# Kernel tuning notes

Measured on AMD Instinct MI355X. Metric: run time of the kernel, lower is better.

Reference implementation:

```python
import jax, jax.numpy as jnp
import numpy as np

N = 100000      # nodes
E = 1600000     # edges
G = 1024        # graphs in batch
NF = 9          # atom features (OGB AtomEncoder)
V = 128         # vocab per atom feature
H = 128         # hidden_dim
L = 3           # num_graph_layers
OUT = 10        # output_dim
BN_EPS = 1e-5


def setup_inputs() -> dict:
    key = jax.random.key(0)
    ks = jax.random.split(key, 12)
    x = jax.random.randint(ks[0], (N, NF), 0, V, dtype=jnp.int32)
    edge_index = jax.random.randint(ks[1], (2, E), 0, N, dtype=jnp.int32)
    batch = jnp.sort(jax.random.randint(ks[2], (N,), 0, G, dtype=jnp.int32))
    emb = jax.random.normal(ks[3], (NF, V, H), dtype=jnp.float32) * 0.05
    Ws = jax.random.normal(ks[4], (L, H, H), dtype=jnp.float32) * (1.0 / np.sqrt(H))
    bs = jnp.zeros((L, H), dtype=jnp.float32)
    gamma = jnp.ones((L - 1, H), dtype=jnp.float32)
    beta = jnp.zeros((L - 1, H), dtype=jnp.float32)
    run_mean = jax.random.normal(ks[5], (L - 1, H), dtype=jnp.float32) * 0.1
    run_var = jax.random.uniform(ks[6], (L - 1, H), minval=0.5, maxval=1.5, dtype=jnp.float32)
    W_clf = jax.random.normal(ks[7], (H, OUT), dtype=jnp.float32) * (1.0 / np.sqrt(H))
    b_clf = jnp.zeros((OUT,), dtype=jnp.float32)
    return {"x": x, "edge_index": edge_index, "batch": batch, "emb": emb,
            "Ws": Ws, "bs": bs, "gamma": gamma, "beta": beta,
            "run_mean": run_mean, "run_var": run_var,
            "W_clf": W_clf, "b_clf": b_clf}


def reference(x, edge_index, batch, emb, Ws, bs, gamma, beta, run_mean, run_var, W_clf, b_clf):
    # Eval-mode forward: dropout = identity, BatchNorm uses running stats.
    src, dst = edge_index[0], edge_index[1]
    # GCN symmetric normalization with self-loops: deg = 1 + in-degree
    deg = jax.ops.segment_sum(jnp.ones((E,), jnp.float32), dst, num_segments=N) + 1.0
    dinv = jax.lax.rsqrt(deg)                 # [N]
    norm_e = dinv[src] * dinv[dst]            # [E] edge coefficient
    norm_self = dinv * dinv                   # [N] self-loop coefficient

    # AtomEncoder: sum of per-feature embedding lookups -> [N, H]
    h = emb[jnp.arange(NF)[None, :], x].sum(axis=1)

    for i in range(L):
        hw = h @ Ws[i]                                                       # [N, H]
        h = (jax.ops.segment_sum(hw[src] * norm_e[:, None], dst, num_segments=N)
             + hw * norm_self[:, None] + bs[i])                              # GCNConv
        if i < L - 1:
            h = (h - run_mean[i]) * (gamma[i] * jax.lax.rsqrt(run_var[i] + BN_EPS)) + beta[i]
            h = jax.nn.relu(h)

    # global mean pool over graphs
    counts = jax.ops.segment_sum(jnp.ones((N,), jnp.float32), batch, num_segments=G)
    pooled = jax.ops.segment_sum(h, batch, num_segments=G) / jnp.maximum(counts, 1.0)[:, None]
    return pooled @ W_clf + b_clf             # [G, OUT]
```

## Files before the change

### kernel.cpp

```cpp
#include <hip/hip_runtime.h>
#include <hip/hip_bf16.h>
#include <hip/hip_fp16.h>

#define NN 100000
#define EE 1600000
#define GG 1024
#define NF 9
#define VV 128
#define HH 128
#define LL 3
#define OUTD 10
#define BN_EPS 1e-5f
#define NBUCK 196
#define BCAP 12288
#define CHUNK 4096
#define NSPLIT 391
#define NENC 3125
#define NB128 782

typedef __attribute__((ext_vector_type(8))) short short8;
typedef __attribute__((ext_vector_type(4))) float f32x4;

__device__ inline unsigned short f2bf(float x) {
    unsigned u = __float_as_uint(x);
    unsigned r = (u + 0x7fffu + ((u >> 16) & 1u)) >> 16;
    return (unsigned short)r;
}
__device__ inline float bf2f(unsigned short b) { return __uint_as_float(((unsigned)b) << 16); }

__device__ inline void mix8(float a[8], const uint4& r, float nm) {
    asm("v_fma_mix_f32 %0, %8, %12, %0 op_sel:[0,0,0] op_sel_hi:[1,0,0]\n\t"
        "v_fma_mix_f32 %1, %8, %12, %1 op_sel:[1,0,0] op_sel_hi:[1,0,0]\n\t"
        "v_fma_mix_f32 %2, %9, %12, %2 op_sel:[0,0,0] op_sel_hi:[1,0,0]\n\t"
        "v_fma_mix_f32 %3, %9, %12, %3 op_sel:[1,0,0] op_sel_hi:[1,0,0]\n\t"
        "v_fma_mix_f32 %4, %10, %12, %4 op_sel:[0,0,0] op_sel_hi:[1,0,0]\n\t"
        "v_fma_mix_f32 %5, %10, %12, %5 op_sel:[1,0,0] op_sel_hi:[1,0,0]\n\t"
        "v_fma_mix_f32 %6, %11, %12, %6 op_sel:[0,0,0] op_sel_hi:[1,0,0]\n\t"
        "v_fma_mix_f32 %7, %11, %12, %7 op_sel:[1,0,0] op_sel_hi:[1,0,0]"
        : "+v"(a[0]), "+v"(a[1]), "+v"(a[2]), "+v"(a[3]),
          "+v"(a[4]), "+v"(a[5]), "+v"(a[6]), "+v"(a[7])
        : "v"(r.x), "v"(r.y), "v"(r.z), "v"(r.w), "v"(nm));
}

__global__ __launch_bounds__(256) void wprep_kernel(const float* __restrict__ Ws,
        const float* __restrict__ Wc, const float* __restrict__ b2,
        unsigned short* __restrict__ WThi, unsigned short* __restrict__ WTlo,
        unsigned short* __restrict__ WcThi, unsigned short* __restrict__ WcTlo,
        float* __restrict__ bb2, int* __restrict__ bcur, float* __restrict__ pooled) {
    int id = blockIdx.x * 256 + threadIdx.x;
    if (id < LL * HH * HH) {
        int layer = id >> 14;
        int rem = id & (HH * HH - 1);
        int k = rem >> 7, n = rem & 127;
        float w = Ws[id];
        unsigned short hi = f2bf(w);
        float lo = w - bf2f(hi);
        WThi[(size_t)layer * HH * HH + n * HH + k] = hi;
        WTlo[(size_t)layer * HH * HH + n * HH + k] = f2bf(lo);
    }
    int tid = threadIdx.x;
    if (blockIdx.x == 0) {
        const float* W2 = Ws + (size_t)2 * HH * HH;
        for (int i = tid; i < 16 * HH; i += 256) {
            int n = i >> 7, k = i & 127;
            float s = 0.f;
            if (n < OUTD) {
                for (int j = 0; j < HH; ++j)
                    s += W2[k * HH + j] * Wc[j * OUTD + n];
            }
            unsigned short hi = f2bf(s);
            WcThi[i] = hi;
            WcTlo[i] = f2bf(s - bf2f(hi));
        }
        if (tid < OUTD) {
            float s = 0.f;
            for (int c = 0; c < HH; ++c) s += b2[c] * Wc[c * OUTD + tid];
            bb2[tid] = s;
        }
    } else if (blockIdx.x == 1) {
        bcur[tid] = 0;
    } else if (blockIdx.x >= 2 && blockIdx.x < 66) {
        pooled[(blockIdx.x - 2) * 256 + tid] = 0.f;
    }
}

__global__ __launch_bounds__(256) void split_enc_kernel(
        const int* __restrict__ src, const int* __restrict__ dst,
        int* __restrict__ bcur, int* __restrict__ bucket_edges,
        const int* __restrict__ x, const float* __restrict__ emb,
        const unsigned short* __restrict__ WThi, const unsigned short* __restrict__ WTlo,
        __half* __restrict__ hw_out) {
    __shared__ __align__(16) char smem_raw[25600];
    int tid = threadIdx.x;
    if (blockIdx.x < NSPLIT) {
        int* lcnt  = (int*)smem_raw;
        int* loff  = lcnt + 256;
        int* lcur  = loff + 256;
        int* gbase = lcur + 256;
        int* sh    = gbase + 256;
        int* stage = sh + 256;
        unsigned char* stageb = (unsigned char*)(stage + CHUNK);
        int cs = blockIdx.x * CHUNK;
        int n = min(CHUNK, EE - cs);
        lcnt[tid] = 0;
        __syncthreads();
        for (int i = tid; i < n; i += 256)
            atomicAdd(&lcnt[dst[cs + i] >> 9], 1);
        __syncthreads();
        int val = lcnt[tid];
        sh[tid] = val; __syncthreads();
        for (int d = 1; d < 256; d <<= 1) {
            int t = (tid >= d) ? sh[tid - d] : 0;
            __syncthreads();
            sh[tid] += t;
            __syncthreads();
        }
        loff[tid] = sh[tid] - val;
        lcur[tid] = sh[tid] - val;
        __syncthreads();
        for (int i = tid; i < n; i += 256) {
            int d = dst[cs + i], s = src[cs + i];
            int b = d >> 9;
            int p = atomicAdd(&lcur[b], 1);
            stage[p] = (s << 9) | (d & 511);
            stageb[p] = (unsigned char)b;
        }
        if (val > 0) gbase[tid] = atomicAdd(&bcur[tid], val);
        __syncthreads();
        for (int i = tid; i < n; i += 256) {
            int b = stageb[i];
            bucket_edges[(size_t)b * BCAP + gbase[b] + (i - loff[b])] = stage[i];
        }
    } else {
        unsigned short (*lh)[136] = (unsigned short(*)[136])smem_raw;
        unsigned short (*ll)[136] = (unsigned short(*)[136])(smem_raw + 32 * 136 * 2);
        int nloc = tid >> 3;
        int seg = tid & 7;
        int nodebase = (blockIdx.x - NSPLIT) * 32;
        int n = nodebase + nloc;
        float s[16];
#pragma unroll
        for (int i = 0; i < 16; ++i) s[i] = 0.f;
#pragma unroll
        for (int f = 0; f < NF; ++f) {
            int idx = x[n * NF + f];
            const float4* ep = (const float4*)(emb + ((size_t)(f * VV + idx)) * HH + seg * 16);
#pragma unroll
            for (int q = 0; q < 4; ++q) {
                float4 e = ep[q];
                s[q * 4 + 0] += e.x; s[q * 4 + 1] += e.y;
                s[q * 4 + 2] += e.z; s[q * 4 + 3] += e.w;
            }
        }
#pragma unroll
        for (int q = 0; q < 4; ++q) {
            ushort4 oh, ol;
            oh.x = f2bf(s[q * 4 + 0]); ol.x = f2bf(s[q * 4 + 0] - bf2f(oh.x));
            oh.y = f2bf(s[q * 4 + 1]); ol.y = f2bf(s[q * 4 + 1] - bf2f(oh.y));
            oh.z = f2bf(s[q * 4 + 2]); ol.z = f2bf(s[q * 4 + 2] - bf2f(oh.z));
            oh.w = f2bf(s[q * 4 + 3]); ol.w = f2bf(s[q * 4 + 3] - bf2f(oh.w));
            *(ushort4*)&lh[nloc][seg * 16 + q * 4] = oh;
            *(ushort4*)&ll[nloc][seg * 16 + q * 4] = ol;
        }
        __syncthreads();
        int wave = tid >> 6, lane = tid & 63;
        int quad = lane >> 4, m = lane & 15;
        f32x4 acc[2][2] = {};
        int kq = quad * 8;
#pragma unroll
        for (int t = 0; t < 4; ++t) {
            int k0 = t * 32 + kq;
            short8 a0h = *(const short8*)&lh[m][k0];
            short8 a0l = *(const short8*)&ll[m][k0];
            short8 a1h = *(const short8*)&lh[16 + m][k0];
            short8 a1l = *(const short8*)&ll[16 + m][k0];
#pragma unroll
            for (int c = 0; c < 2; ++c) {
                int ct = wave * 2 + c;
                short8 bh = *(const short8*)(WThi + (size_t)(ct * 16 + m) * HH + k0);
                short8 bl = *(const short8*)(WTlo + (size_t)(ct * 16 + m) * HH + k0);
                acc[0][c] = __builtin_amdgcn_mfma_f32_16x16x32_bf16(a0h, bh, acc[0][c], 0, 0, 0);
                acc[0][c] = __builtin_amdgcn_mfma_f32_16x16x32_bf16(a0l, bh, acc[0][c], 0, 0, 0);
                acc[0][c] = __builtin_amdgcn_mfma_f32_16x16x32_bf16(a0h, bl, acc[0][c], 0, 0, 0);
                acc[1][c] = __builtin_amdgcn_mfma_f32_16x16x32_bf16(a1h, bh, acc[1][c], 0, 0, 0);
                acc[1][c] = __builtin_amdgcn_mfma_f32_16x16x32_bf16(a1l, bh, acc[1][c], 0, 0, 0);
                acc[1][c] = __builtin_amdgcn_mfma_f32_16x16x32_bf16(a1h, bl, acc[1][c], 0, 0, 0);
            }
        }
#pragma unroll
        for (int c = 0; c < 2; ++c) {
            int colx = (wave * 2 + c) * 16 + m;
#pragma unroll
            for (int rt = 0; rt < 2; ++rt) {
                int r0 = nodebase + rt * 16 + quad * 4;
#pragma unroll
                for (int reg = 0; reg < 4; ++reg)
                    hw_out[(size_t)(r0 + reg) * HH + colx] = __float2half(acc[rt][c][reg]);
            }
        }
    }
}

__global__ __launch_bounds__(256) void bhist_kernel(const int* __restrict__ bcur,
                                                    const int* __restrict__ bucket_edges,
                                                    int* __restrict__ cnt,
                                                    float* __restrict__ dinv,
                                                    int* __restrict__ bsum) {
    __shared__ int lc[512];
    __shared__ int sh[256];
    int b = blockIdx.x, tid = threadIdx.x;
    lc[tid] = 0; lc[tid + 256] = 0;
    __syncthreads();
    int n = bcur[b];
    const int* be = bucket_edges + (size_t)b * BCAP;
    for (int i = tid; i < n; i += 256) atomicAdd(&lc[be[i] & 511], 1);
    __syncthreads();
    int node = b * 512 + tid;
    int c0 = lc[tid], c1 = lc[tid + 256];
    int s = 0;
    if (node < NN) { cnt[node] = c0; dinv[node] = rsqrtf(1.0f + (float)c0); s += c0; }
    if (node + 256 < NN) { cnt[node + 256] = c1; dinv[node + 256] = rsqrtf(1.0f + (float)c1); s += c1; }
    sh[tid] = s; __syncthreads();
    for (int d = 128; d > 0; d >>= 1) { if (tid < d) sh[tid] += sh[tid + d]; __syncthreads(); }
    if (tid == 0) bsum[b] = sh[0];
}

__global__ void scanC_kernel(const int* __restrict__ cnt, const int* __restrict__ bsum,
                             int* __restrict__ row_ptr) {
    __shared__ int sh[256];
    __shared__ int pre[256];
    int tid = threadIdx.x;
    pre[tid] = (tid < blockIdx.x && tid < NBUCK) ? bsum[tid] : 0;
    __syncthreads();
    for (int d = 128; d > 0; d >>= 1) { if (tid < d) pre[tid] += pre[tid + d]; __syncthreads(); }
    int bbase = pre[0];
    int base = blockIdx.x * 512 + tid * 2;
    int v0 = (base < NN) ? cnt[base] : 0;
    int v1 = (base + 1 < NN) ? cnt[base + 1] : 0;
    int ts = v0 + v1;
    sh[tid] = ts; __syncthreads();
    for (int d = 1; d < 256; d <<= 1) {
        int t = (tid >= d) ? sh[tid - d] : 0;
        __syncthreads();
        sh[tid] += t;
        __syncthreads();
    }
    int excl = sh[tid] - ts + bbase;
    if (base < NN) row_ptr[base] = excl;
    if (base + 1 < NN) row_ptr[base + 1] = excl + v0;
    if (blockIdx.x == 0 && tid == 0) row_ptr[NN] = EE;
}

__global__ __launch_bounds__(256) void cscatter_kernel(const int* __restrict__ bcur,
                                                       const int* __restrict__ bucket_edges,
                                                       const int* __restrict__ row_ptr,
                                                       const float* __restrict__ dinv,
                                                       int2* __restrict__ col) {
    __shared__ int lcur[512];
    int b = blockIdx.x, tid = threadIdx.x;
    int node0 = b * 512;
#pragma unroll
    for (int k = 0; k < 2; ++k) {
        int j = tid + k * 256;
        int node = node0 + j;
        if (node < NN) lcur[j] = row_ptr[node];
    }
    __syncthreads();
    int n = bcur[b];
    const int* be = bucket_edges + (size_t)b * BCAP;
    for (int i = tid; i < n; i += 256) {
        int w = be[i];
        int j = w & 511;
        int s = (int)((unsigned)w >> 9);
        int p = atomicAdd(&lcur[j], 1);
        float nm = dinv[s] * dinv[node0 + j];
        col[p] = make_int2(s, __float_as_int(nm));
    }
}

__device__ inline void gather_node(const uint4* __restrict__ hw4,
                                   const int2* __restrict__ col,
                                   int start, int end, int c4,
                                   float a[8], float b[8]) {
    int e = start;
    for (; e + 4 <= end; e += 4) {
        unsigned long long w0 = *(const unsigned long long*)&col[e];
        unsigned long long w1 = *(const unsigned long long*)&col[e + 1];
        unsigned long long w2 = *(const unsigned long long*)&col[e + 2];
        unsigned long long w3 = *(const unsigned long long*)&col[e + 3];
        uint4 r0 = hw4[(size_t)(unsigned)(w0 & 0xffffffffu) * 16 + c4];
        uint4 r1 = hw4[(size_t)(unsigned)(w1 & 0xffffffffu) * 16 + c4];
        uint4 r2 = hw4[(size_t)(unsigned)(w2 & 0xffffffffu) * 16 + c4];
        uint4 r3 = hw4[(size_t)(unsigned)(w3 & 0xffffffffu) * 16 + c4];
        mix8(a, r0, __int_as_float((int)(unsigned)(w0 >> 32)));
        mix8(b, r1, __int_as_float((int)(unsigned)(w1 >> 32)));
        mix8(a, r2, __int_as_float((int)(unsigned)(w2 >> 32)));
        mix8(b, r3, __int_as_float((int)(unsigned)(w3 >> 32)));
    }
    if (e < end) {
        int last = end - 1;
        int e1 = min(e + 1, last), e2 = min(e + 2, last), e3 = min(e + 3, last);
        unsigned long long w0 = *(const unsigned long long*)&col[e];
        unsigned long long w1 = *(const unsigned long long*)&col[e1];
        unsigned long long w2 = *(const unsigned long long*)&col[e2];
        unsigned long long w3 = *(const unsigned long long*)&col[e3];
        float n0 = __int_as_float((int)(unsigned)(w0 >> 32));
        float n1 = (e + 1 < end) ? __int_as_float((int)(unsigned)(w1 >> 32)) : 0.f;
        float n2 = (e + 2 < end) ? __int_as_float((int)(unsigned)(w2 >> 32)) : 0.f;
        float n3 = (e + 3 < end) ? __int_as_float((int)(unsigned)(w3 >> 32)) : 0.f;
        uint4 r0 = hw4[(size_t)(unsigned)(w0 & 0xffffffffu) * 16 + c4];
        uint4 r1 = hw4[(size_t)(unsigned)(w1 & 0xffffffffu) * 16 + c4];
        uint4 r2 = hw4[(size_t)(unsigned)(w2 & 0xffffffffu) * 16 + c4];
        uint4 r3 = hw4[(size_t)(unsigned)(w3 & 0xffffffffu) * 16 + c4];
        mix8(a, r0, n0);
        mix8(b, r1, n1);
        mix8(a, r2, n2);
        mix8(b, r3, n3);
    }
}

template<bool DO_PROJ>
__global__ __launch_bounds__(512) void agg_mm_kernel(const __half* __restrict__ hw_in,
    const int* __restrict__ row_ptr, const int2* __restrict__ col,
    const float* __restrict__ dinv,
    const float* __restrict__ bias, const float* __restrict__ gamma,
    const float* __restrict__ beta, const float* __restrict__ rmean,
    const float* __restrict__ rvar,
    const unsigned short* __restrict__ WThi, const unsigned short* __restrict__ WTlo,
    __half* __restrict__ hw_out,
    const unsigned short* __restrict__ WcThi, const unsigned short* __restrict__ WcTlo,
    __half* __restrict__ y_out) {
    __shared__ __align__(16) unsigned short lh[32][136];
    __shared__ __align__(16) unsigned short ll[32][136];
    int wave = threadIdx.x >> 6;
    int lane = threadIdx.x & 63;
    int grp = lane >> 4;
    int c4 = lane & 15;
    int nodebase = blockIdx.x * 32;
    const uint4* hw4 = (const uint4*)hw_in;

    int v = nodebase + wave * 4 + grp;
    int start = row_ptr[v], end = row_ptr[v + 1];
    float a[8] = {}, b[8] = {};
    gather_node(hw4, col, start, end, c4, a, b);

    {
        float dv = dinv[v];
        uint4 r = hw4[(size_t)v * 16 + c4];
        mix8(a, r, dv * dv);
    }
#pragma unroll
    for (int i = 0; i < 8; ++i) a[i] += b[i];

    int ch = c4 * 8;
#pragma unroll
    for (int i = 0; i < 8; ++i) a[i] += bias[ch + i];
#pragma unroll
    for (int i = 0; i < 8; ++i) {
        int c = ch + i;
        float sc = gamma[c] * rsqrtf(rvar[c] + BN_EPS);
        a[i] = fmaxf((a[i] - rmean[c]) * sc + beta[c], 0.f);
    }
    int rloc = wave * 4 + grp;
    ushort4 oh0, oh1, ol0, ol1;
    oh0.x = f2bf(a[0]); ol0.x = f2bf(a[0] - bf2f(oh0.x));
    oh0.y = f2bf(a[1]); ol0.y = f2bf(a[1] - bf2f(oh0.y));
    oh0.z = f2bf(a[2]); ol0.z = f2bf(a[2] - bf2f(oh0.z));
    oh0.w = f2bf(a[3]); ol0.w = f2bf(a[3] - bf2f(oh0.w));
    oh1.x = f2bf(a[4]); ol1.x = f2bf(a[4] - bf2f(oh1.x));
    oh1.y = f2bf(a[5]); ol1.y = f2bf(a[5] - bf2f(oh1.y));
    oh1.z = f2bf(a[6]); ol1.z = f2bf(a[6] - bf2f(oh1.z));
    oh1.w = f2bf(a[7]); ol1.w = f2bf(a[7] - bf2f(oh1.w));
    *(ushort4*)&lh[rloc][ch]     = oh0;
    *(ushort4*)&lh[rloc][ch + 4] = oh1;
    *(ushort4*)&ll[rloc][ch]     = ol0;
    *(ushort4*)&ll[rloc][ch + 4] = ol1;

    __syncthreads();
    int quad = lane >> 4, m = lane & 15;
    f32x4 acc[2] = {};
    int kq = quad * 8;
    int ct = wave;
#pragma unroll
    for (int t = 0; t < 4; ++t) {
        int k0 = t * 32 + kq;
        short8 a0h = *(const short8*)&lh[m][k0];
        short8 a0l = *(const short8*)&ll[m][k0];
        short8 a1h = *(const short8*)&lh[16 + m][k0];
        short8 a1l = *(const short8*)&ll[16 + m][k0];
        short8 bh = *(const short8*)(WThi + (size_t)(ct * 16 + m) * HH + k0);
        short8 bl = *(const short8*)(WTlo + (size_t)(ct * 16 + m) * HH + k0);
        acc[0] = __builtin_amdgcn_mfma_f32_16x16x32_bf16(a0h, bh, acc[0], 0, 0, 0);
        acc[0] = __builtin_amdgcn_mfma_f32_16x16x32_bf16(a0l, bh, acc[0], 0, 0, 0);
        acc[0] = __builtin_amdgcn_mfma_f32_16x16x32_bf16(a0h, bl, acc[0], 0, 0, 0);
        acc[1] = __builtin_amdgcn_mfma_f32_16x16x32_bf16(a1h, bh, acc[1], 0, 0, 0);
        acc[1] = __builtin_amdgcn_mfma_f32_16x16x32_bf16(a1l, bh, acc[1], 0, 0, 0);
        acc[1] = __builtin_amdgcn_mfma_f32_16x16x32_bf16(a1h, bl, acc[1], 0, 0, 0);
    }
    int colx = ct * 16 + m;
#pragma unroll
    for (int rt = 0; rt < 2; ++rt) {
        int r0 = nodebase + rt * 16 + quad * 4;
#pragma unroll
        for (int reg = 0; reg < 4; ++reg)
            hw_out[(size_t)(r0 + reg) * HH + colx] = __float2half(acc[rt][reg]);
    }

    if constexpr (DO_PROJ) {
        if (wave < 2) {
            f32x4 pacc = {};
#pragma unroll
            for (int t = 0; t < 4; ++t) {
                int k0 = t * 32 + kq;
                short8 ah = *(const short8*)&lh[wave * 16 + m][k0];
                short8 al = *(const short8*)&ll[wave * 16 + m][k0];
                short8 bh = *(const short8*)(WcThi + (size_t)m * HH + k0);
                short8 bl = *(const short8*)(WcTlo + (size_t)m * HH + k0);
                pacc = __builtin_amdgcn_mfma_f32_16x16x32_bf16(ah, bh, pacc, 0, 0, 0);
                pacc = __builtin_amdgcn_mfma_f32_16x16x32_bf16(al, bh, pacc, 0, 0, 0);
                pacc = __builtin_amdgcn_mfma_f32_16x16x32_bf16(ah, bl, pacc, 0, 0, 0);
            }
#pragma unroll
            for (int reg = 0; reg < 4; ++reg) {
                int node = nodebase + wave * 16 + quad * 4 + reg;
                y_out[(size_t)node * 16 + m] = __float2half(pacc[reg]);
            }
        }
    }
}

__global__ __launch_bounds__(256) void agg_pool_kernel(const __half* __restrict__ y,
    const int* __restrict__ row_ptr, const int2* __restrict__ col,
    const float* __restrict__ dinv, const int* __restrict__ batch,
    float* __restrict__ pooled) {
    __shared__ __align__(16) float lz[128][16];
    __shared__ int bg[128];
    int tid = threadIdx.x;
    int g2 = tid >> 1;
    int cl = tid & 1;
    int nodebase = blockIdx.x * 128;
    int v = nodebase + g2;
    int vc = min(v, NN - 1);
    int start = row_ptr[vc];
    int end = (v < NN) ? row_ptr[vc + 1] : start;
    const uint4* y4 = (const uint4*)y;
    float a[8] = {};
    int e = start;
    for (; e + 4 <= end; e += 4) {
        unsigned long long w0 = *(const unsigned long long*)&col[e];
        unsigned long long w1 = *(const unsigned long long*)&col[e + 1];
        unsigned long long w2 = *(const unsigned long long*)&col[e + 2];
        unsigned long long w3 = *(const unsigned long long*)&col[e + 3];
        uint4 r0 = y4[(size_t)(unsigned)(w0 & 0xffffffffu) * 2 + cl];
        uint4 r1 = y4[(size_t)(unsigned)(w1 & 0xffffffffu) * 2 + cl];
        uint4 r2 = y4[(size_t)(unsigned)(w2 & 0xffffffffu) * 2 + cl];
        uint4 r3 = y4[(size_t)(unsigned)(w3 & 0xffffffffu) * 2 + cl];
        mix8(a, r0, __int_as_float((int)(unsigned)(w0 >> 32)));
        mix8(a, r1, __int_as_float((int)(unsigned)(w1 >> 32)));
        mix8(a, r2, __int_as_float((int)(unsigned)(w2 >> 32)));
        mix8(a, r3, __int_as_float((int)(unsigned)(w3 >> 32)));
    }
    if (e < end) {
        int last = end - 1;
        int e1 = min(e + 1, last), e2 = min(e + 2, last), e3 = min(e + 3, last);
        unsigned long long w0 = *(const unsigned long long*)&col[e];
        unsigned long long w1 = *(const unsigned long long*)&col[e1];
        unsigned long long w2 = *(const unsigned long long*)&col[e2];
        unsigned long long w3 = *(const unsigned long long*)&col[e3];
        float n0 = __int_as_float((int)(unsigned)(w0 >> 32));
        float n1 = (e + 1 < end) ? __int_as_float((int)(unsigned)(w1 >> 32)) : 0.f;
        float n2 = (e + 2 < end) ? __int_as_float((int)(unsigned)(w2 >> 32)) : 0.f;
        float n3 = (e + 3 < end) ? __int_as_float((int)(unsigned)(w3 >> 32)) : 0.f;
        uint4 r0 = y4[(size_t)(unsigned)(w0 & 0xffffffffu) * 2 + cl];
        uint4 r1 = y4[(size_t)(unsigned)(w1 & 0xffffffffu) * 2 + cl];
        uint4 r2 = y4[(size_t)(unsigned)(w2 & 0xffffffffu) * 2 + cl];
        uint4 r3 = y4[(size_t)(unsigned)(w3 & 0xffffffffu) * 2 + cl];
        mix8(a, r0, n0);
        mix8(a, r1, n1);
        mix8(a, r2, n2);
        mix8(a, r3, n3);
    }
    if (v < NN) {
        float dv = dinv[v];
        uint4 r = y4[(size_t)v * 2 + cl];
        mix8(a, r, dv * dv);
    } else {
#pragma unroll
        for (int i = 0; i < 8; ++i) a[i] = 0.f;
    }
    int chb = cl * 8;
#pragma unroll
    for (int i = 0; i < 8; ++i) lz[g2][chb + i] = a[i];
    if (cl == 0) bg[g2] = batch[vc];
    __syncthreads();
    int ch = tid & 15;
    int rh = tid >> 4;
    int r0i = rh * 8;
    int curg = bg[r0i];
    float run = 0.f;
    for (int r = r0i; r < r0i + 8; ++r) {
        int gg = bg[r];
        if (gg != curg) {
            atomicAdd(&pooled[(size_t)curg * 16 + ch], run);
            run = 0.f; curg = gg;
        }
        run += lz[r][ch];
    }
    atomicAdd(&pooled[(size_t)curg * 16 + ch], run);
}

__global__ __launch_bounds__(256) void finalize_kernel(const float* __restrict__ pooled,
    const int* __restrict__ batch, const float* __restrict__ bb2,
    const float* __restrict__ bc, float* __restrict__ out) {
    int id = blockIdx.x * 256 + threadIdx.x;
    if (id >= GG * 16) return;
    int g = id >> 4, o = id & 15;
    if (o >= OUTD) return;
    int lo = 0, hi = NN;
    while (lo < hi) { int mid = (lo + hi) >> 1; if (batch[mid] < g) lo = mid + 1; else hi = mid; }
    int s0 = lo;
    lo = 0; hi = NN;
    int g1 = g + 1;
    while (lo < hi) { int mid = (lo + hi) >> 1; if (batch[mid] < g1) lo = mid + 1; else hi = mid; }
    int cnt = lo - s0;
    float r = pooled[(size_t)g * 16 + o] / fmaxf((float)cnt, 1.0f);
    out[(size_t)g * OUTD + o] = r + ((cnt > 0) ? bb2[o] : 0.f) + bc[o];
}

extern "C" void kernel_launch(void* const* d_in, const int* in_sizes, int n_in,
                              void* d_out, int out_size, void* d_ws, size_t ws_size,
                              hipStream_t stream) {
    const int*   x      = (const int*)d_in[0];
    const int*   eidx   = (const int*)d_in[1];
    const int*   batch  = (const int*)d_in[2];
    const float* emb    = (const float*)d_in[3];
    const float* Ws     = (const float*)d_in[4];
    const float* bs     = (const float*)d_in[5];
    const float* gamma  = (const float*)d_in[6];
    const float* beta   = (const float*)d_in[7];
    const float* rmean  = (const float*)d_in[8];
    const float* rvar   = (const float*)d_in[9];
    const float* Wclf   = (const float*)d_in[10];
    const float* bclf   = (const float*)d_in[11];
    float* out = (float*)d_out;

    const int* e_src = eidx;
    const int* e_dst = eidx + EE;

    char* ws = (char*)d_ws;
    size_t off = 0;
    auto take = [&](size_t bytes) -> void* {
        void* p = ws + off;
        off = (off + bytes + 255) & ~(size_t)255;
        return p;
    };
    float* dinv     = (float*)take((size_t)NN * 4);
    int*   cnt      = (int*)  take((size_t)NN * 4);
    int*   row_ptr  = (int*)  take((size_t)(NN + 1) * 4);
    int*   bsum     = (int*)  take((size_t)NBUCK * 4);
    int*   bcur     = (int*)  take((size_t)256 * 4);
    int*   bucket_edges = (int*)take((size_t)NBUCK * BCAP * 4);
    int2*  col      = (int2*) take((size_t)EE * 8 + 64);
    __half* hwA     = (__half*)take((size_t)NN * HH * 2);
    __half* hwB     = (__half*)take((size_t)NN * HH * 2);
    __half* yh      = (__half*)take((size_t)NN * 16 * 2);
    float* pooled   = (float*)take((size_t)GG * 16 * 4);
    unsigned short* WThi = (unsigned short*)take((size_t)LL * HH * HH * 2);
    unsigned short* WTlo = (unsigned short*)take((size_t)LL * HH * HH * 2);
    unsigned short* WcThi = (unsigned short*)take((size_t)16 * HH * 2);
    unsigned short* WcTlo = (unsigned short*)take((size_t)16 * HH * 2);
    float* bb2      = (float*)take((size_t)16 * 4);

    wprep_kernel<<<(LL * HH * HH + 255) / 256, 256, 0, stream>>>(Ws, Wclf, bs + 2 * HH,
        WThi, WTlo, WcThi, WcTlo, bb2, bcur, pooled);
    split_enc_kernel<<<NSPLIT + NENC, 256, 0, stream>>>(e_src, e_dst, bcur, bucket_edges,
        x, emb, WThi, WTlo, hwA);
    bhist_kernel<<<NBUCK, 256, 0, stream>>>(bcur, bucket_edges, cnt, dinv, bsum);
    scanC_kernel<<<NBUCK, 256, 0, stream>>>(cnt, bsum, row_ptr);
    cscatter_kernel<<<NBUCK, 256, 0, stream>>>(bcur, bucket_edges, row_ptr, dinv, col);

    agg_mm_kernel<false><<<NN / 32, 512, 0, stream>>>(hwA, row_ptr, col, dinv,
        bs, gamma, beta, rmean, rvar,
        WThi + (size_t)1 * HH * HH, WTlo + (size_t)1 * HH * HH, hwB,
        nullptr, nullptr, nullptr);
    agg_mm_kernel<true><<<NN / 32, 512, 0, stream>>>(hwB, row_ptr, col, dinv,
        bs + HH, gamma + HH, beta + HH, rmean + HH, rvar + HH,
        WThi + (size_t)2 * HH * HH, WTlo + (size_t)2 * HH * HH, hwA,
        WcThi, WcTlo, yh);
    agg_pool_kernel<<<NB128, 256, 0, stream>>>(yh, row_ptr, col, dinv, batch, pooled);
    finalize_kernel<<<(GG * 16 + 255) / 256, 256, 0, stream>>>(pooled, batch, bb2, bclf, out);
}
```

Before: 394.7 us.

## Split hidden features into 16-channel slices and separate gather from BN+matmul

Stores the projected hidden states in a sliced layout (8 slices of 16 channels per node) so each gather block reads only one 32-byte slice per neighbour, which should improve cache locality of the random edge gathers. The fused aggregate+matmul kernel is split into a gather kernel that writes fp32 aggregates to a new buffer and a separate BN/ReLU+MFMA kernel. This removes the wide 256-byte row gathers but adds a full fp32 round trip of N×128 values through memory and extra launches, and the col/row_ptr arrays are reread once per slice.

```diff
diff --git a/kernel.cpp b/kernel.cpp
--- a/kernel.cpp
+++ b/kernel.cpp
@@ -17,6 +17,8 @@
 #define NSPLIT 391
 #define NENC 3125
 #define NB128 782
+#define NSL 8
+#define SLN ((size_t)NN * 16)
 
 typedef __attribute__((ext_vector_type(8))) short short8;
 typedef __attribute__((ext_vector_type(4))) float f32x4;
@@ -189,13 +191,14 @@
         }
 #pragma unroll
         for (int c = 0; c < 2; ++c) {
-            int colx = (wave * 2 + c) * 16 + m;
+            int ct = wave * 2 + c;
 #pragma unroll
             for (int rt = 0; rt < 2; ++rt) {
                 int r0 = nodebase + rt * 16 + quad * 4;
 #pragma unroll
                 for (int reg = 0; reg < 4; ++reg)
-                    hw_out[(size_t)(r0 + reg) * HH + colx] = __float2half(acc[rt][c][reg]);
+                    hw_out[(size_t)ct * SLN + (size_t)(r0 + reg) * 16 + m] =
+                        __float2half(acc[rt][c][reg]);
             }
         }
     }
@@ -278,24 +281,33 @@
     }
 }
 
-__device__ inline void gather_node(const uint4* __restrict__ hw4,
-                                   const int2* __restrict__ col,
-                                   int start, int end, int c4,
-                                   float a[8], float b[8]) {
+__global__ __launch_bounds__(256) void gather16_kernel(const __half* __restrict__ hw_s,
+    const int* __restrict__ row_ptr, const int2* __restrict__ col,
+    const float* __restrict__ dinv, float* __restrict__ aggbuf) {
+    int slice = blockIdx.x & 7;
+    int nblk = blockIdx.x >> 3;
+    int tid = threadIdx.x;
+    int g2 = tid >> 1, cl = tid & 1;
+    int v = nblk * 128 + g2;
+    int vc = min(v, NN - 1);
+    int start = row_ptr[vc];
+    int end = (v < NN) ? row_ptr[vc + 1] : start;
+    const uint4* hb = (const uint4*)hw_s + (size_t)slice * (NN * 2);
+    float a[8] = {};
     int e = start;
     for (; e + 4 <= end; e += 4) {
         unsigned long long w0 = *(const unsigned long long*)&col[e];
         unsigned long long w1 = *(const unsigned long long*)&col[e + 1];
         unsigned long long w2 = *(const unsigned long long*)&col[e + 2];
         unsigned long long w3 = *(const unsigned long long*)&col[e + 3];
-        uint4 r0 = hw4[(size_t)(unsigned)(w0 & 0xffffffffu) * 16 + c4];
-        uint4 r1 = hw4[(size_t)(unsigned)(w1 & 0xffffffffu) * 16 + c4];
-        uint4 r2 = hw4[(size_t)(unsigned)(w2 & 0xffffffffu) * 16 + c4];
-        uint4 r3 = hw4[(size_t)(unsigned)(w3 & 0xffffffffu) * 16 + c4];
+        uint4 r0 = hb[(size_t)(unsigned)(w0 & 0xffffffffu) * 2 + cl];
+        uint4 r1 = hb[(size_t)(unsigned)(w1 & 0xffffffffu) * 2 + cl];
+        uint4 r2 = hb[(size_t)(unsigned)(w2 & 0xffffffffu) * 2 + cl];
+        uint4 r3 = hb[(size_t)(unsigned)(w3 & 0xffffffffu) * 2 + cl];
         mix8(a, r0, __int_as_float((int)(unsigned)(w0 >> 32)));
-        mix8(b, r1, __int_as_float((int)(unsigned)(w1 >> 32)));
+        mix8(a, r1, __int_as_float((int)(unsigned)(w1 >> 32)));
         mix8(a, r2, __int_as_float((int)(unsigned)(w2 >> 32)));
-        mix8(b, r3, __int_as_float((int)(unsigned)(w3 >> 32)));
+        mix8(a, r3, __int_as_float((int)(unsigned)(w3 >> 32)));
     }
     if (e < end) {
         int last = end - 1;
@@ -308,105 +320,103 @@
         float n1 = (e + 1 < end) ? __int_as_float((int)(unsigned)(w1 >> 32)) : 0.f;
         float n2 = (e + 2 < end) ? __int_as_float((int)(unsigned)(w2 >> 32)) : 0.f;
         float n3 = (e + 3 < end) ? __int_as_float((int)(unsigned)(w3 >> 32)) : 0.f;
-        uint4 r0 = hw4[(size_t)(unsigned)(w0 & 0xffffffffu) * 16 + c4];
-        uint4 r1 = hw4[(size_t)(unsigned)(w1 & 0xffffffffu) * 16 + c4];
-        uint4 r2 = hw4[(size_t)(unsigned)(w2 & 0xffffffffu) * 16 + c4];
-        uint4 r3 = hw4[(size_t)(unsigned)(w3 & 0xffffffffu) * 16 + c4];
+        uint4 r0 = hb[(size_t)(unsigned)(w0 & 0xffffffffu) * 2 + cl];
+        uint4 r1 = hb[(size_t)(unsigned)(w1 & 0xffffffffu) * 2 + cl];
+        uint4 r2 = hb[(size_t)(unsigned)(w2 & 0xffffffffu) * 2 + cl];
+        uint4 r3 = hb[(size_t)(unsigned)(w3 & 0xffffffffu) * 2 + cl];
         mix8(a, r0, n0);
-        mix8(b, r1, n1);
+        mix8(a, r1, n1);
         mix8(a, r2, n2);
-        mix8(b, r3, n3);
-    }
-}
-
-template<bool DO_PROJ>
-__global__ __launch_bounds__(512) void agg_mm_kernel(const __half* __restrict__ hw_in,
-    const int* __restrict__ row_ptr, const int2* __restrict__ col,
-    const float* __restrict__ dinv,
+        mix8(a, r3, n3);
+    }
+    if (v < NN) {
+        float dv = dinv[v];
+        uint4 r = hb[(size_t)v * 2 + cl];
+        mix8(a, r, dv * dv);
+        float4* o = (float4*)(aggbuf + ((size_t)slice * NN + v) * 16 + cl * 8);
+        o[0] = make_float4(a[0], a[1], a[2], a[3]);
+        o[1] = make_float4(a[4], a[5], a[6], a[7]);
+    }
+}
+
+template<int MODE>
+__global__ __launch_bounds__(256) void bn_mm_kernel(const float* __restrict__ aggbuf,
     const float* __restrict__ bias, const float* __restrict__ gamma,
     const float* __restrict__ beta, const float* __restrict__ rmean,
     const float* __restrict__ rvar,
     const unsigned short* __restrict__ WThi, const unsigned short* __restrict__ WTlo,
-    __half* __restrict__ hw_out,
-    const unsigned short* __restrict__ WcThi, const unsigned short* __restrict__ WcTlo,
-    __half* __restrict__ y_out) {
+    __half* __restrict__ out_h) {
     __shared__ __align__(16) unsigned short lh[32][136];
     __shared__ __align__(16) unsigned short ll[32][136];
-    int wave = threadIdx.x >> 6;
-    int lane = threadIdx.x & 63;
-    int grp = lane >> 4;
-    int c4 = lane & 15;
+    int tid = threadIdx.x;
+    int nloc = tid >> 3;
+    int seg = tid & 7;
     int nodebase = blockIdx.x * 32;
-    const uint4* hw4 = (const uint4*)hw_in;
-
-    int v = nodebase + wave * 4 + grp;
-    int start = row_ptr[v], end = row_ptr[v + 1];
-    float a[8] = {}, b[8] = {};
-    gather_node(hw4, col, start, end, c4, a, b);
-
-    {
-        float dv = dinv[v];
-        uint4 r = hw4[(size_t)v * 16 + c4];
-        mix8(a, r, dv * dv);
-    }
-#pragma unroll
-    for (int i = 0; i < 8; ++i) a[i] += b[i];
-
-    int ch = c4 * 8;
-#pragma unroll
-    for (int i = 0; i < 8; ++i) a[i] += bias[ch + i];
-#pragma unroll
-    for (int i = 0; i < 8; ++i) {
-        int c = ch + i;
+    int n = nodebase + nloc;
+    const float4* ap = (const float4*)(aggbuf + ((size_t)seg * NN + n) * 16);
+    float s[16];
+#pragma unroll
+    for (int q = 0; q < 4; ++q) {
+        float4 e = ap[q];
+        s[q * 4 + 0] = e.x; s[q * 4 + 1] = e.y;
+        s[q * 4 + 2] = e.z; s[q * 4 + 3] = e.w;
+    }
+    int chb = seg * 16;
+#pragma unroll
+    for (int i = 0; i < 16; ++i) {
+        int c = chb + i;
         float sc = gamma[c] * rsqrtf(rvar[c] + BN_EPS);
-        a[i] = fmaxf((a[i] - rmean[c]) * sc + beta[c], 0.f);
-    }
-    int rloc = wave * 4 + grp;
-    ushort4 oh0, oh1, ol0, ol1;
-    oh0.x = f2bf(a[0]); ol0.x = f2bf(a[0] - bf2f(oh0.x));
-    oh0.y = f2bf(a[1]); ol0.y = f2bf(a[1] - bf2f(oh0.y));
-    oh0.z = f2bf(a[2]); ol0.z = f2bf(a[2] - bf2f(oh0.z));
-    oh0.w = f2bf(a[3]); ol0.w = f2bf(a[3] - bf2f(oh0.w));
-    oh1.x = f2bf(a[4]); ol1.x = f2bf(a[4] - bf2f(oh1.x));
-    oh1.y = f2bf(a[5]); ol1.y = f2bf(a[5] - bf2f(oh1.y));
-    oh1.z = f2bf(a[6]); ol1.z = f2bf(a[6] - bf2f(oh1.z));
-    oh1.w = f2bf(a[7]); ol1.w = f2bf(a[7] - bf2f(oh1.w));
-    *(ushort4*)&lh[rloc][ch]     = oh0;
-    *(ushort4*)&lh[rloc][ch + 4] = oh1;
-    *(ushort4*)&ll[rloc][ch]     = ol0;
-    *(ushort4*)&ll[rloc][ch + 4] = ol1;
-
+        s[i] = fmaxf((s[i] + bias[c] - rmean[c]) * sc + beta[c], 0.f);
+    }
+#pragma unroll
+    for (int q = 0; q < 4; ++q) {
+        ushort4 oh, ol;
+        oh.x = f2bf(s[q * 4 + 0]); ol.x = f2bf(s[q * 4 + 0] - bf2f(oh.x));
+        oh.y = f2bf(s[q * 4 + 1]); ol.y = f2bf(s[q * 4 + 1] - bf2f(oh.y));
+        oh.z = f2bf(s[q * 4 + 2]); ol.z = f2bf(s[q * 4 + 2] - bf2f(oh.z));
+        oh.w = f2bf(s[q * 4 + 3]); ol.w = f2bf(s[q * 4 + 3] - bf2f(oh.w));
+        *(ushort4*)&lh[nloc][chb + q * 4] = oh;
+        *(ushort4*)&ll[nloc][chb + q * 4] = ol;
+    }
     __syncthreads();
+    int wave = tid >> 6, lane = tid & 63;
     int quad = lane >> 4, m = lane & 15;
-    f32x4 acc[2] = {};
     int kq = quad * 8;
-    int ct = wave;
-#pragma unroll
-    for (int t = 0; t < 4; ++t) {
-        int k0 = t * 32 + kq;
-        short8 a0h = *(const short8*)&lh[m][k0];
-        short8 a0l = *(const short8*)&ll[m][k0];
-        short8 a1h = *(const short8*)&lh[16 + m][k0];
-        short8 a1l = *(const short8*)&ll[16 + m][k0];
-        short8 bh = *(const short8*)(WThi + (size_t)(ct * 16 + m) * HH + k0);
-        short8 bl = *(const short8*)(WTlo + (size_t)(ct * 16 + m) * HH + k0);
-        acc[0] = __builtin_amdgcn_mfma_f32_16x16x32_bf16(a0h, bh, acc[0], 0, 0, 0);
-        acc[0] = __builtin_amdgcn_mfma_f32_16x16x32_bf16(a0l, bh, acc[0], 0, 0, 0);
-        acc[0] = __builtin_amdgcn_mfma_f32_16x16x32_bf16(a0h, bl, acc[0], 0, 0, 0);
-        acc[1] = __builtin_amdgcn_mfma_f32_16x16x32_bf16(a1h, bh, acc[1], 0, 0, 0);
-        acc[1] = __builtin_amdgcn_mfma_f32_16x16x32_bf16(a1l, bh, acc[1], 0, 0, 0);
-        acc[1] = __builtin_amdgcn_mfma_f32_16x16x32_bf16(a1h, bl, acc[1], 0, 0, 0);
-    }
-    int colx = ct * 16 + m;
-#pragma unroll
-    for (int rt = 0; rt < 2; ++rt) {
-        int r0 = nodebase + rt * 16 + quad * 4;
-#pragma unroll
-        for (int reg = 0; reg < 4; ++reg)
-            hw_out[(size_t)(r0 + reg) * HH + colx] = __float2half(acc[rt][reg]);
-    }
-
-    if constexpr (DO_PROJ) {
+    if constexpr (MODE == 0) {
+        f32x4 acc[2][2] = {};
+#pragma unroll
+        for (int t = 0; t < 4; ++t) {
+            int k0 = t * 32 + kq;
+            short8 a0h = *(const short8*)&lh[m][k0];
+            short8 a0l = *(const short8*)&ll[m][k0];
+            short8 a1h = *(const short8*)&lh[16 + m][k0];
+            short8 a1l = *(const short8*)&ll[16 + m][k0];
+#pragma unroll
+            for (int c = 0; c < 2; ++c) {
+                int ct = wave * 2 + c;
+                short8 bh = *(const short8*)(WThi + (size_t)(ct * 16 + m) * HH + k0);
+                short8 bl = *(const short8*)(WTlo + (size_t)(ct * 16 + m) * HH + k0);
+                acc[0][c] = __builtin_amdgcn_mfma_f32_16x16x32_bf16(a0h, bh, acc[0][c], 0, 0, 0);
+                acc[0][c] = __builtin_amdgcn_mfma_f32_16x16x32_bf16(a0l, bh, acc[0][c], 0, 0, 0);
+                acc[0][c] = __builtin_amdgcn_mfma_f32_16x16x32_bf16(a0h, bl, acc[0][c], 0, 0, 0);
+                acc[1][c] = __builtin_amdgcn_mfma_f32_16x16x32_bf16(a1h, bh, acc[1][c], 0, 0, 0);
+                acc[1][c] = __builtin_amdgcn_mfma_f32_16x16x32_bf16(a1l, bh, acc[1][c], 0, 0, 0);
+                acc[1][c] = __builtin_amdgcn_mfma_f32_16x16x32_bf16(a1h, bl, acc[1][c], 0, 0, 0);
+            }
+        }
+#pragma unroll
+        for (int c = 0; c < 2; ++c) {
+            int ct = wave * 2 + c;
+#pragma unroll
+            for (int rt = 0; rt < 2; ++rt) {
+                int r0 = nodebase + rt * 16 + quad * 4;
+#pragma unroll
+                for (int reg = 0; reg < 4; ++reg)
+                    out_h[(size_t)ct * SLN + (size_t)(r0 + reg) * 16 + m] =
+                        __float2half(acc[rt][c][reg]);
+            }
+        }
+    } else {
         if (wave < 2) {
             f32x4 pacc = {};
 #pragma unroll
@@ -414,8 +424,8 @@
                 int k0 = t * 32 + kq;
                 short8 ah = *(const short8*)&lh[wave * 16 + m][k0];
                 short8 al = *(const short8*)&ll[wave * 16 + m][k0];
-                short8 bh = *(const short8*)(WcThi + (size_t)m * HH + k0);
-                short8 bl = *(const short8*)(WcTlo + (size_t)m * HH + k0);
+                short8 bh = *(const short8*)(WThi + (size_t)m * HH + k0);
+                short8 bl = *(const short8*)(WTlo + (size_t)m * HH + k0);
                 pacc = __builtin_amdgcn_mfma_f32_16x16x32_bf16(ah, bh, pacc, 0, 0, 0);
                 pacc = __builtin_amdgcn_mfma_f32_16x16x32_bf16(al, bh, pacc, 0, 0, 0);
                 pacc = __builtin_amdgcn_mfma_f32_16x16x32_bf16(ah, bl, pacc, 0, 0, 0);
@@ -423,7 +433,7 @@
 #pragma unroll
             for (int reg = 0; reg < 4; ++reg) {
                 int node = nodebase + wave * 16 + quad * 4 + reg;
-                y_out[(size_t)node * 16 + m] = __float2half(pacc[reg]);
+                out_h[(size_t)node * 16 + m] = __float2half(pacc[reg]);
             }
         }
     }
@@ -564,6 +574,7 @@
     __half* hwA     = (__half*)take((size_t)NN * HH * 2);
     __half* hwB     = (__half*)take((size_t)NN * HH * 2);
     __half* yh      = (__half*)take((size_t)NN * 16 * 2);
+    float* aggbuf   = (float*)take((size_t)NN * HH * 4);
     float* pooled   = (float*)take((size_t)GG * 16 * 4);
     unsigned short* WThi = (unsigned short*)take((size_t)LL * HH * HH * 2);
     unsigned short* WTlo = (unsigned short*)take((size_t)LL * HH * HH * 2);
@@ -579,13 +590,13 @@
     scanC_kernel<<<NBUCK, 256, 0, stream>>>(cnt, bsum, row_ptr);
     cscatter_kernel<<<NBUCK, 256, 0, stream>>>(bcur, bucket_edges, row_ptr, dinv, col);
 
-    agg_mm_kernel<false><<<NN / 32, 512, 0, stream>>>(hwA, row_ptr, col, dinv,
+    gather16_kernel<<<NSL * NB128, 256, 0, stream>>>(hwA, row_ptr, col, dinv, aggbuf);
+    bn_mm_kernel<0><<<NN / 32, 256, 0, stream>>>(aggbuf,
         bs, gamma, beta, rmean, rvar,
-        WThi + (size_t)1 * HH * HH, WTlo + (size_t)1 * HH * HH, hwB,
-        nullptr, nullptr, nullptr);
-    agg_mm_kernel<true><<<NN / 32, 512, 0, stream>>>(hwB, row_ptr, col, dinv,
+        WThi + (size_t)1 * HH * HH, WTlo + (size_t)1 * HH * HH, hwB);
+    gather16_kernel<<<NSL * NB128, 256, 0, stream>>>(hwB, row_ptr, col, dinv, aggbuf);
+    bn_mm_kernel<1><<<NN / 32, 256, 0, stream>>>(aggbuf,
         bs + HH, gamma + HH, beta + HH, rmean + HH, rvar + HH,
-        WThi + (size_t)2 * HH * HH, WTlo + (size_t)2 * HH * HH, hwA,
         WcThi, WcTlo, yh);
     agg_pool_kernel<<<NB128, 256, 0, stream>>>(yh, row_ptr, col, dinv, batch, pooled);
     finalize_kernel<<<(GG * 16 + 255) / 256, 256, 0, stream>>>(pooled, batch, bb2, bclf, out);
```

After: 526.9 us. 1.34x slower.
